# Kernel optimization log

Hardware: AMD Instinct MI355X
Metric: run time of the kernel (lower is better)

The kernel has to match this reference:

```python
import jax, jax.numpy as jnp
import numpy as np

NUM_HEADS = 8
HEAD_DIM = 96  # dim_out // num_heads = 768 // 8
DIM_OUT = 768
STRIDE = 2


def setup_inputs() -> dict:
    key = jax.random.key(0)
    k1, k2, k3, k4, k5 = jax.random.split(key, 5)
    B, H, W, C = 4, 64, 64, 384
    hidden_states = jax.random.normal(k1, (B, H, W, C), dtype=jnp.float32)
    qkv_w = jax.random.normal(k2, (C, 3 * DIM_OUT), dtype=jnp.float32) * (C ** -0.5)
    qkv_b = jax.random.normal(k3, (3 * DIM_OUT,), dtype=jnp.float32) * 0.02
    proj_w = jax.random.normal(k4, (DIM_OUT, DIM_OUT), dtype=jnp.float32) * (DIM_OUT ** -0.5)
    proj_b = jax.random.normal(k5, (DIM_OUT,), dtype=jnp.float32) * 0.02
    return {"hidden_states": hidden_states, "qkv_w": qkv_w, "qkv_b": qkv_b,
            "proj_w": proj_w, "proj_b": proj_b}


def reference(hidden_states, qkv_w, qkv_b, proj_w, proj_b):
    B, H, W, C = hidden_states.shape
    scale = HEAD_DIM ** -0.5
    # QKV projection over channels
    qkv = jnp.einsum('bhwc,cd->bhwd', hidden_states, qkv_w) + qkv_b  # [B,H,W,3*Do]
    qkv = qkv.reshape(B, H * W, 3, NUM_HEADS, HEAD_DIM)
    q, k, v = qkv[:, :, 0], qkv[:, :, 1], qkv[:, :, 2]  # [B, HW, nh, hd]
    # Max-pool queries spatially by STRIDE
    q = q.reshape(B, H, W, DIM_OUT)
    Hq, Wq = H // STRIDE, W // STRIDE
    q = q.reshape(B, Hq, STRIDE, Wq, STRIDE, DIM_OUT).max(axis=(2, 4))  # [B,Hq,Wq,Do]
    q = q.reshape(B, Hq * Wq, NUM_HEADS, HEAD_DIM)
    # Attention: Lq = Hq*Wq, Lk = H*W
    attn = jnp.einsum('bqhd,bkhd->bhqk', q * scale, k)
    attn = jax.nn.softmax(attn, axis=-1)
    out = jnp.einsum('bhqk,bkhd->bqhd', attn, v)  # [B,Lq,nh,hd]
    out = out.reshape(B, Hq, Wq, DIM_OUT)
    out = jnp.einsum('bhwc,cd->bhwd', out, proj_w) + proj_b
    return out
```

## Files before the change

### kernel.cpp

```cpp
#include <hip/hip_runtime.h>
#include <hip/hip_bf16.h>

typedef unsigned short u16;
typedef __attribute__((ext_vector_type(8))) short bf16x8;
typedef __attribute__((ext_vector_type(8))) unsigned short u16x8;
typedef __attribute__((ext_vector_type(4))) float f32x4;

#define MFMA16(a,b,c) __builtin_amdgcn_mfma_f32_16x16x32_bf16(a,b,c,0,0,0)

__device__ __forceinline__ u16 f2bf(float f) {
  union { float f; unsigned int u; } v; v.f = f;
  unsigned int r = v.u + 0x7fffu + ((v.u >> 16) & 1u);
  return (u16)(r >> 16);
}
__device__ __forceinline__ float bf2f(u16 u) {
  union { unsigned int i; float f; } v; v.i = ((unsigned int)u) << 16; return v.f;
}

__device__ __forceinline__ void gld16(const void* g, void* l) {
  __builtin_amdgcn_global_load_lds((const __attribute__((address_space(1))) void*)g,
                                   (__attribute__((address_space(3))) void*)l, 16, 0, 0);
}

__device__ __forceinline__ void ttrans_body(const float* __restrict__ in, u16* __restrict__ out,
                                            int K, int N, int blk, int tid, u16 T[64][65]) {
  const int ntx = N >> 6;
  const int tx = blk % ntx, ty = blk / ntx;
  const int n0 = tx * 64, k0 = ty * 64;
  #pragma unroll
  for (int p = 0; p < 4; ++p) {
    int idx = p * 256 + tid;
    int r = idx >> 4, ch = idx & 15;
    float4 v = *reinterpret_cast<const float4*>(in + (size_t)(k0 + r) * N + n0 + ch * 4);
    T[r][ch * 4 + 0] = f2bf(v.x);
    T[r][ch * 4 + 1] = f2bf(v.y);
    T[r][ch * 4 + 2] = f2bf(v.z);
    T[r][ch * 4 + 3] = f2bf(v.w);
  }
  __syncthreads();
  #pragma unroll
  for (int p = 0; p < 2; ++p) {
    int idx = p * 256 + tid;
    int rr = idx >> 3, ch = idx & 7;
    u16x8 o;
    #pragma unroll
    for (int e = 0; e < 8; ++e) o[e] = T[ch * 8 + e][rr];
    *reinterpret_cast<u16x8*>(out + (size_t)(n0 + rr) * K + k0 + ch * 8) = o;
  }
}

__global__ void prep(const float* __restrict__ hs, u16* __restrict__ hs_bf,
                     const float* __restrict__ qkv_w, u16* __restrict__ qkvwT,
                     const float* __restrict__ proj_w, u16* __restrict__ projwT) {
  __shared__ u16 T[64][65];
  const int blk = blockIdx.x, tid = threadIdx.x;
  if (blk < 6144) {
    int i = blk * 256 + tid;
    float4 v = reinterpret_cast<const float4*>(hs)[i];
    ushort4 o; o.x = f2bf(v.x); o.y = f2bf(v.y); o.z = f2bf(v.z); o.w = f2bf(v.w);
    reinterpret_cast<ushort4*>(hs_bf)[i] = o;
  } else if (blk < 6360) {
    ttrans_body(qkv_w, qkvwT, 384, 2304, blk - 6144, tid, T);
  } else {
    ttrans_body(proj_w, projwT, 768, 768, blk - 6360, tid, T);
  }
}

template<int EPI>
__launch_bounds__(256)
__global__ void gemm_bt(const u16* __restrict__ A, const u16* __restrict__ Bt,
                        const float* __restrict__ bias,
                        u16* __restrict__ qp, u16* __restrict__ ok, u16* __restrict__ ov,
                        float* __restrict__ of, int K, int nbx, int cpx) {
  __shared__ __align__(16) u16 Sh[16384];
  const int id = blockIdx.x;
  const int id2 = (id & 7) * cpx + (id >> 3);
  const int bx = id2 % nbx, by = id2 / nbx;
  const int tid = threadIdx.x;
  const int wave = tid >> 6, lane = tid & 63;
  const int c = lane & 15, g = lane >> 4;
  const int brow = by * 128, bcol = bx * 128;
  const int wr = (wave >> 1) * 64, wc = (wave & 1) * 64;
  f32x4 acc[4][4] = {};
  const int srow = wave * 32 + (lane >> 2);
  const int scol = (lane & 3) * 8;
  const u16* agp0 = A  + (size_t)(brow + srow) * K + scol;
  const u16* agp1 = A  + (size_t)(brow + srow + 16) * K + scol;
  const u16* bgp0 = Bt + (size_t)(bcol + srow) * K + scol;
  const u16* bgp1 = Bt + (size_t)(bcol + srow + 16) * K + scol;
  const int lo0 = wave * 1024, lo1 = wave * 1024 + 512;
  const int nk = K >> 5;
  gld16(agp0, &Sh[lo0]);
  gld16(agp1, &Sh[lo1]);
  gld16(bgp0, &Sh[8192 + lo0]);
  gld16(bgp1, &Sh[8192 + lo1]);
  for (int ks = 0; ks < nk; ++ks) {
    const int cur = ks & 1;
    if (ks + 1 < nk) {
      const int k1 = (ks + 1) << 5;
      const int nb = (cur ^ 1) * 4096;
      gld16(agp0 + k1, &Sh[nb + lo0]);
      gld16(agp1 + k1, &Sh[nb + lo1]);
      gld16(bgp0 + k1, &Sh[8192 + nb + lo0]);
      gld16(bgp1 + k1, &Sh[8192 + nb + lo1]);
      asm volatile("s_waitcnt vmcnt(4)" ::: "memory");
    } else {
      asm volatile("s_waitcnt vmcnt(0)" ::: "memory");
    }
    __builtin_amdgcn_s_barrier();
    __builtin_amdgcn_sched_barrier(0);
    const int cb = cur * 4096;
    bf16x8 af[4], bfr[4];
    #pragma unroll
    for (int mi = 0; mi < 4; ++mi)
      af[mi] = *reinterpret_cast<const bf16x8*>(&Sh[cb + (wr + mi * 16 + c) * 32 + g * 8]);
    #pragma unroll
    for (int ni = 0; ni < 4; ++ni)
      bfr[ni] = *reinterpret_cast<const bf16x8*>(&Sh[8192 + cb + (wc + ni * 16 + c) * 32 + g * 8]);
    #pragma unroll
    for (int mi = 0; mi < 4; ++mi)
      #pragma unroll
      for (int ni = 0; ni < 4; ++ni)
        acc[mi][ni] = MFMA16(af[mi], bfr[ni], acc[mi][ni]);
    __builtin_amdgcn_sched_barrier(0);
    __builtin_amdgcn_s_barrier();
  }
  if (EPI == 0 && bcol < 768) {
    const float SC = 0.14724744f;
    float* P = (float*)&Sh[0];
    float m01[4][4], m23[4][4];
    #pragma unroll
    for (int mi = 0; mi < 4; ++mi)
      #pragma unroll
      for (int ni = 0; ni < 4; ++ni) {
        m01[mi][ni] = fmaxf(acc[mi][ni][0], acc[mi][ni][1]);
        m23[mi][ni] = fmaxf(acc[mi][ni][2], acc[mi][ni][3]);
      }
    if (wr == 64) {
      #pragma unroll
      for (int mi = 0; mi < 4; ++mi)
        #pragma unroll
        for (int ni = 0; ni < 4; ++ni) {
          const int pw = mi * 8 + g * 2;
          P[(wave & 1) * 2048 + pw * 64 + ni * 16 + c]       = m01[mi][ni];
          P[(wave & 1) * 2048 + (pw + 1) * 64 + ni * 16 + c] = m23[mi][ni];
        }
    }
    __syncthreads();
    if (wr == 0) {
      const int b = brow >> 12;
      const int hq = (brow >> 7) & 31;
      const size_t rbase = (size_t)(b * 1024 + hq * 32);
      #pragma unroll
      for (int mi = 0; mi < 4; ++mi)
        #pragma unroll
        for (int ni = 0; ni < 4; ++ni) {
          const int col = bcol + wc + ni * 16 + c;
          const float bz = bias[col];
          const int pw = mi * 8 + g * 2;
          float v0 = fmaxf(m01[mi][ni], P[(wave & 1) * 2048 + pw * 64 + ni * 16 + c]);
          float v1 = fmaxf(m23[mi][ni], P[(wave & 1) * 2048 + (pw + 1) * 64 + ni * 16 + c]);
          qp[(rbase + pw) * 768 + col]     = f2bf((v0 + bz) * SC);
          qp[(rbase + pw + 1) * 768 + col] = f2bf((v1 + bz) * SC);
        }
    }
    return;
  }
  if (EPI == 0 && bcol >= 1536) {
    u16* T = &Sh[0];
    const int vc0 = bcol - 1536;
    const int bq = brow >> 12;
    const int s0 = brow & 4095;
    #pragma unroll
    for (int ni = 0; ni < 4; ++ni) {
      const int j = wc + ni * 16 + c;
      const float bz = bias[bcol + j];
      const int key = (j & 15) << 2;
      #pragma unroll
      for (int mi = 0; mi < 4; ++mi) {
        const int rb = wr + mi * 16 + g * 4;
        ushort4 o;
        o.x = f2bf(acc[mi][ni][0] + bz);
        o.y = f2bf(acc[mi][ni][1] + bz);
        o.z = f2bf(acc[mi][ni][2] + bz);
        o.w = f2bf(acc[mi][ni][3] + bz);
        *reinterpret_cast<ushort4*>(&T[j * 128 + (rb ^ key)]) = o;
      }
    }
    __syncthreads();
    u16* vb2 = ov + ((size_t)(bq * 768 + vc0)) * 4096 + s0;
    #pragma unroll
    for (int p = 0; p < 8; ++p) {
      const int j = p * 16 + wave * 4 + (lane >> 4);
      const int sc = lane & 15;
      const int key = j & 15;
      const int p4 = 8 * (sc >> 3) + 2 * (sc & 3) + ((sc >> 2) & 1);
      uint2 lo = *reinterpret_cast<uint2*>(&T[j * 128 + ((sc ^ key) << 2)]);
      uint2 hi = *reinterpret_cast<uint2*>(&T[j * 128 + (((sc + 16) ^ key) << 2)]);
      *reinterpret_cast<uint2*>(vb2 + (size_t)j * 4096 + p4 * 4)      = lo;
      *reinterpret_cast<uint2*>(vb2 + (size_t)j * 4096 + 64 + p4 * 4) = hi;
    }
    return;
  }
  #pragma unroll
  for (int mi = 0; mi < 4; ++mi) {
    #pragma unroll
    for (int ni = 0; ni < 4; ++ni) {
      const int col = bcol + wc + ni * 16 + c;
      const float bz = bias[col];
      #pragma unroll
      for (int i = 0; i < 4; ++i) {
        const int row = brow + wr + mi * 16 + g * 4 + i;
        float v = acc[mi][ni][i] + bz;
        if (EPI == 0) {
          ok[(size_t)row * 768 + col - 768] = f2bf(v);
        } else {
          of[(size_t)row * 768 + col] = v;
        }
      }
    }
  }
}

__launch_bounds__(512, 4)
__global__ void flash7(const u16* __restrict__ Qp, const u16* __restrict__ Kb,
                       const u16* __restrict__ Vtg, u16* __restrict__ aout) {
  const int blk = blockIdx.x;
  const int xcd = blk & 7, j = blk >> 3;
  const int bh = xcd + 8 * (j >> 4), qt = j & 15;
  const int b = bh >> 3, h = bh & 7;
  __shared__ __align__(16) u16 Sh[24576];
  const int tid = threadIdx.x, w = tid >> 6, lane = tid & 63;
  const int sq = w >> 2, wq = w & 3;
  const int c = lane & 15, g = lane >> 4;
  const int kbase = sq * 12288;
  const int vbase = 6144 + sq * 12288;
  const u16* qb = Qp + ((size_t)(b * 1024 + qt * 64 + wq * 16 + c)) * 768 + h * 96;
  bf16x8 qf[3];
  #pragma unroll
  for (int kc = 0; kc < 3; ++kc)
    qf[kc] = *reinterpret_cast<const bf16x8*>(qb + kc * 32 + g * 8);
  int koff[3], voff[3], loff[3];
  #pragma unroll
  for (int j2 = 0; j2 < 3; ++j2) {
    int p = wq * 192 + j2 * 64 + lane;
    int r = p / 12, ch = p - r * 12;
    koff[j2] = r * 768 + ch * 8;
    int d = p >> 3, vch = p & 7;
    voff[j2] = d * 4096 + ((vch ^ (d & 7)) * 8);
    loff[j2] = (wq * 192 + j2 * 64) * 8;
  }
  const u16* kb0 = Kb + ((size_t)(b * 4096 + sq * 2048)) * 768 + h * 96;
  const u16* vb0 = Vtg + ((size_t)(bh * 96)) * 4096 + sq * 2048;
  float m = -1e30f, l = 0.f;
  f32x4 acc[6] = {};
  const int sw = (c & 7) << 3;
  for (int kt = 0; kt < 32; ++kt) {
    __syncthreads();
    #pragma unroll
    for (int j2 = 0; j2 < 3; ++j2) gld16(kb0 + (size_t)kt * 49152 + koff[j2], &Sh[kbase + loff[j2]]);
    #pragma unroll
    for (int j2 = 0; j2 < 3; ++j2) gld16(vb0 + kt * 64 + voff[j2], &Sh[vbase + loff[j2]]);
    __syncthreads();
    f32x4 st[4] = {};
    #pragma unroll
    for (int kc = 0; kc < 3; ++kc)
      #pragma unroll
      for (int kt4 = 0; kt4 < 4; ++kt4) {
        bf16x8 kf = *reinterpret_cast<const bf16x8*>(&Sh[kbase + (kt4 * 16 + c) * 96 + kc * 32 + g * 8]);
        st[kt4] = MFMA16(kf, qf[kc], st[kt4]);
      }
    float pmax = st[0][0];
    #pragma unroll
    for (int kt4 = 0; kt4 < 4; ++kt4)
      #pragma unroll
      for (int i = 0; i < 4; ++i)
        pmax = fmaxf(pmax, st[kt4][i]);
    pmax = fmaxf(pmax, __shfl_xor(pmax, 16));
    pmax = fmaxf(pmax, __shfl_xor(pmax, 32));
    if (__any(pmax > m + 8.0f)) {
      float mn = fmaxf(m, pmax);
      float esc = exp2f(m - mn);
      m = mn;
      l *= esc;
      float er[4];
      #pragma unroll
      for (int i = 0; i < 4; ++i) er[i] = __shfl(esc, g * 4 + i);
      #pragma unroll
      for (int dc = 0; dc < 6; ++dc)
        #pragma unroll
        for (int i = 0; i < 4; ++i)
          acc[dc][i] *= er[i];
    }
    float ps = 0.f;
    #pragma unroll
    for (int kt4 = 0; kt4 < 4; ++kt4)
      #pragma unroll
      for (int i = 0; i < 4; ++i) {
        float p = exp2f(st[kt4][i] - m);
        st[kt4][i] = p;
        ps += p;
      }
    ps += __shfl_xor(ps, 16);
    ps += __shfl_xor(ps, 32);
    l += ps;
    unsigned int uu[4][2];
    #pragma unroll
    for (int kt4 = 0; kt4 < 4; ++kt4) {
      asm("v_cvt_pk_bf16_f32 %0, %1, %2" : "=v"(uu[kt4][0]) : "v"(st[kt4][0]), "v"(st[kt4][1]));
      asm("v_cvt_pk_bf16_f32 %0, %1, %2" : "=v"(uu[kt4][1]) : "v"(st[kt4][2]), "v"(st[kt4][3]));
    }
    #pragma unroll
    for (int kh = 0; kh < 2; ++kh) {
      union { unsigned int wrd[4]; bf16x8 v; } pfu;
      pfu.wrd[0] = uu[2 * kh][0];
      pfu.wrd[1] = uu[2 * kh][1];
      pfu.wrd[2] = uu[2 * kh + 1][0];
      pfu.wrd[3] = uu[2 * kh + 1][1];
      bf16x8 pf = pfu.v;
      #pragma unroll
      for (int dc = 0; dc < 6; ++dc) {
        bf16x8 vf = *reinterpret_cast<const bf16x8*>(&Sh[vbase + (dc * 16 + c) * 64 + ((kh * 32 + g * 8) ^ sw)]);
        acc[dc] = MFMA16(pf, vf, acc[dc]);
      }
    }
  }
  __syncthreads();
  float* Cb = (float*)&Sh[0];
  float* Ml = (float*)&Sh[12288];
  if (sq == 1) {
    #pragma unroll
    for (int dc = 0; dc < 6; ++dc)
      #pragma unroll
      for (int i = 0; i < 4; ++i)
        Cb[(wq * 16 + g * 4 + i) * 96 + dc * 16 + c] = acc[dc][i];
    if (lane < 16) {
      Ml[(wq * 16 + lane) * 2]     = m;
      Ml[(wq * 16 + lane) * 2 + 1] = l;
    }
  }
  __syncthreads();
  if (sq == 0) {
    u16* ob = aout + (size_t)(b * 1024 + qt * 64 + wq * 16) * 768 + h * 96;
    #pragma unroll
    for (int i = 0; i < 4; ++i) {
      const int q = g * 4 + i;
      float m0q = __shfl(m, q), l0q = __shfl(l, q);
      float m1q = Ml[(wq * 16 + q) * 2], l1q = Ml[(wq * 16 + q) * 2 + 1];
      float M = fmaxf(m0q, m1q);
      float e0 = exp2f(m0q - M), e1 = exp2f(m1q - M);
      float inv = 1.f / (l0q * e0 + l1q * e1);
      #pragma unroll
      for (int dc = 0; dc < 6; ++dc) {
        float a1 = Cb[(wq * 16 + q) * 96 + dc * 16 + c];
        ob[(size_t)q * 768 + dc * 16 + c] = f2bf((acc[dc][i] * e0 + a1 * e1) * inv);
      }
    }
  }
}

extern "C" void kernel_launch(void* const* d_in, const int* in_sizes, int n_in,
                              void* d_out, int out_size, void* d_ws, size_t ws_size,
                              hipStream_t stream) {
  const float* hs     = (const float*)d_in[0];
  const float* qkv_w  = (const float*)d_in[1];
  const float* qkv_b  = (const float*)d_in[2];
  const float* proj_w = (const float*)d_in[3];
  const float* proj_b = (const float*)d_in[4];
  float* out = (float*)d_out;

  u16* hs_bf  = (u16*)d_ws;
  u16* qkvwT  = hs_bf  + 6291456;
  u16* projwT = qkvwT  + 884736;
  u16* vT     = projwT + 589824;
  u16* kbuf   = vT     + 12582912;
  u16* spare  = kbuf   + 12582912;
  u16* qpol   = spare  + 12582912;
  u16* aout   = qpol   + 3145728;

  prep<<<6504, 256, 0, stream>>>(hs, hs_bf, qkv_w, qkvwT, proj_w, projwT);

  gemm_bt<0><<<2304, 256, 0, stream>>>(hs_bf, qkvwT, qkv_b,
                                       qpol, kbuf, vT, nullptr, 384, 18, 288);
  flash7<<<512, 512, 0, stream>>>(qpol, kbuf, vT, aout);
  gemm_bt<1><<<192, 256, 0, stream>>>(aout, projwT, proj_b,
                                      nullptr, nullptr, nullptr, out, 768, 6, 24);
}
```

Measured before the change: 160.6 us.

## Micro-optimize flash kernel: raw exp, max3 reduction, setprio, pointer increments

```diff
diff --git a/kernel.cpp b/kernel.cpp
--- a/kernel.cpp
+++ b/kernel.cpp
@@ -15,6 +15,16 @@
 }
 __device__ __forceinline__ float bf2f(u16 u) {
   union { unsigned int i; float f; } v; v.i = ((unsigned int)u) << 16; return v.f;
+}
+__device__ __forceinline__ float exp2a(float x) {
+  float r;
+  asm("v_exp_f32 %0, %1" : "=v"(r) : "v"(x));
+  return r;
+}
+__device__ __forceinline__ float max3(float a, float b, float c) {
+  float r;
+  asm("v_max3_f32 %0, %1, %2, %3" : "=v"(r) : "v"(a), "v"(b), "v"(c));
+  return r;
 }
 
 __device__ __forceinline__ void gld16(const void* g, void* l) {
@@ -223,7 +233,7 @@
 }
 
 __launch_bounds__(512, 4)
-__global__ void flash7(const u16* __restrict__ Qp, const u16* __restrict__ Kb,
+__global__ void flash8(const u16* __restrict__ Qp, const u16* __restrict__ Kb,
                        const u16* __restrict__ Vtg, u16* __restrict__ aout) {
   const int blk = blockIdx.x;
   const int xcd = blk & 7, j = blk >> 3;
@@ -240,47 +250,64 @@
   #pragma unroll
   for (int kc = 0; kc < 3; ++kc)
     qf[kc] = *reinterpret_cast<const bf16x8*>(qb + kc * 32 + g * 8);
-  int koff[3], voff[3], loff[3];
-  #pragma unroll
-  for (int j2 = 0; j2 < 3; ++j2) {
-    int p = wq * 192 + j2 * 64 + lane;
-    int r = p / 12, ch = p - r * 12;
-    koff[j2] = r * 768 + ch * 8;
-    int d = p >> 3, vch = p & 7;
-    voff[j2] = d * 4096 + ((vch ^ (d & 7)) * 8);
-    loff[j2] = (wq * 192 + j2 * 64) * 8;
-  }
-  const u16* kb0 = Kb + ((size_t)(b * 4096 + sq * 2048)) * 768 + h * 96;
-  const u16* vb0 = Vtg + ((size_t)(bh * 96)) * 4096 + sq * 2048;
+  const u16* kp[3];
+  const u16* vp[3];
+  int loff[3];
+  {
+    const u16* kb0 = Kb + ((size_t)(b * 4096 + sq * 2048)) * 768 + h * 96;
+    const u16* vb0 = Vtg + ((size_t)(bh * 96)) * 4096 + sq * 2048;
+    #pragma unroll
+    for (int j2 = 0; j2 < 3; ++j2) {
+      int p = wq * 192 + j2 * 64 + lane;
+      int r = p / 12, ch = p - r * 12;
+      kp[j2] = kb0 + r * 768 + ch * 8;
+      int d = p >> 3, vch = p & 7;
+      vp[j2] = vb0 + d * 4096 + ((vch ^ (d & 7)) * 8);
+      loff[j2] = (wq * 192 + j2 * 64) * 8;
+    }
+  }
   float m = -1e30f, l = 0.f;
   f32x4 acc[6] = {};
+  const f32x4 z4 = {0.f, 0.f, 0.f, 0.f};
   const int sw = (c & 7) << 3;
   for (int kt = 0; kt < 32; ++kt) {
     __syncthreads();
     #pragma unroll
-    for (int j2 = 0; j2 < 3; ++j2) gld16(kb0 + (size_t)kt * 49152 + koff[j2], &Sh[kbase + loff[j2]]);
-    #pragma unroll
-    for (int j2 = 0; j2 < 3; ++j2) gld16(vb0 + kt * 64 + voff[j2], &Sh[vbase + loff[j2]]);
+    for (int j2 = 0; j2 < 3; ++j2) gld16(kp[j2], &Sh[kbase + loff[j2]]);
+    #pragma unroll
+    for (int j2 = 0; j2 < 3; ++j2) gld16(vp[j2], &Sh[vbase + loff[j2]]);
+    #pragma unroll
+    for (int j2 = 0; j2 < 3; ++j2) { kp[j2] += 49152; vp[j2] += 64; }
     __syncthreads();
-    f32x4 st[4] = {};
-    #pragma unroll
-    for (int kc = 0; kc < 3; ++kc)
+    f32x4 st[4];
+    __builtin_amdgcn_s_setprio(1);
+    #pragma unroll
+    for (int kt4 = 0; kt4 < 4; ++kt4) {
+      bf16x8 kf = *reinterpret_cast<const bf16x8*>(&Sh[kbase + (kt4 * 16 + c) * 96 + g * 8]);
+      st[kt4] = MFMA16(kf, qf[0], z4);
+    }
+    #pragma unroll
+    for (int kc = 1; kc < 3; ++kc)
       #pragma unroll
       for (int kt4 = 0; kt4 < 4; ++kt4) {
         bf16x8 kf = *reinterpret_cast<const bf16x8*>(&Sh[kbase + (kt4 * 16 + c) * 96 + kc * 32 + g * 8]);
         st[kt4] = MFMA16(kf, qf[kc], st[kt4]);
       }
-    float pmax = st[0][0];
-    #pragma unroll
-    for (int kt4 = 0; kt4 < 4; ++kt4)
-      #pragma unroll
-      for (int i = 0; i < 4; ++i)
-        pmax = fmaxf(pmax, st[kt4][i]);
+    __builtin_amdgcn_s_setprio(0);
+    float pmax;
+    {
+      float a0 = max3(st[0][0], st[0][1], st[0][2]);
+      float a1 = max3(st[0][3], st[1][0], st[1][1]);
+      float a2 = max3(st[1][2], st[1][3], st[2][0]);
+      float a3 = max3(st[2][1], st[2][2], st[2][3]);
+      float a4 = max3(st[3][0], st[3][1], st[3][2]);
+      pmax = fmaxf(max3(a0, a1, st[3][3]), max3(a2, a3, a4));
+    }
     pmax = fmaxf(pmax, __shfl_xor(pmax, 16));
     pmax = fmaxf(pmax, __shfl_xor(pmax, 32));
     if (__any(pmax > m + 8.0f)) {
       float mn = fmaxf(m, pmax);
-      float esc = exp2f(m - mn);
+      float esc = exp2a(m - mn);
       m = mn;
       l *= esc;
       float er[4];
@@ -297,7 +324,7 @@
     for (int kt4 = 0; kt4 < 4; ++kt4)
       #pragma unroll
       for (int i = 0; i < 4; ++i) {
-        float p = exp2f(st[kt4][i] - m);
+        float p = exp2a(st[kt4][i] - m);
         st[kt4][i] = p;
         ps += p;
       }
@@ -310,6 +337,7 @@
       asm("v_cvt_pk_bf16_f32 %0, %1, %2" : "=v"(uu[kt4][0]) : "v"(st[kt4][0]), "v"(st[kt4][1]));
       asm("v_cvt_pk_bf16_f32 %0, %1, %2" : "=v"(uu[kt4][1]) : "v"(st[kt4][2]), "v"(st[kt4][3]));
     }
+    __builtin_amdgcn_s_setprio(1);
     #pragma unroll
     for (int kh = 0; kh < 2; ++kh) {
       union { unsigned int wrd[4]; bf16x8 v; } pfu;
@@ -324,6 +352,7 @@
         acc[dc] = MFMA16(pf, vf, acc[dc]);
       }
     }
+    __builtin_amdgcn_s_setprio(0);
   }
   __syncthreads();
   float* Cb = (float*)&Sh[0];
@@ -348,7 +377,7 @@
       float m0q = __shfl(m, q), l0q = __shfl(l, q);
       float m1q = Ml[(wq * 16 + q) * 2], l1q = Ml[(wq * 16 + q) * 2 + 1];
       float M = fmaxf(m0q, m1q);
-      float e0 = exp2f(m0q - M), e1 = exp2f(m1q - M);
+      float e0 = exp2a(m0q - M), e1 = exp2a(m1q - M);
       float inv = 1.f / (l0q * e0 + l1q * e1);
       #pragma unroll
       for (int dc = 0; dc < 6; ++dc) {
@@ -382,7 +411,7 @@
 
   gemm_bt<0><<<2304, 256, 0, stream>>>(hs_bf, qkvwT, qkv_b,
                                        qpol, kbuf, vT, nullptr, 384, 18, 288);
-  flash7<<<512, 512, 0, stream>>>(qpol, kbuf, vT, aout);
+  flash8<<<512, 512, 0, stream>>>(qpol, kbuf, vT, aout);
   gemm_bt<1><<<192, 256, 0, stream>>>(aout, projwT, proj_b,
                                       nullptr, nullptr, nullptr, out, 768, 6, 24);
 }
```

After: 146.8 us. 1.09x faster.
